# Performance work log

Measured on AMD Instinct MI355X. Metric: run time of the kernel, lower is better.

Reference implementation:

```python
import jax, jax.numpy as jnp
import numpy as np
from jax import lax

E = 20          # num experts / classes
BN_EPS = 1e-5


def _conv(x, w, b=None):
    # NCHW conv, stride 1, 'same' padding (kernel 3x3 or 1x1)
    y = lax.conv_general_dilated(x, w, (1, 1), 'SAME',
                                 dimension_numbers=('NCHW', 'OIHW', 'NCHW'))
    return y if b is None else y + b[None, :, None, None]


def _lrelu(x):
    return jnp.where(x >= 0, x, 0.2 * x)


def _bn(x, g, b, m, v):
    # inference-mode batchnorm
    scale = g * lax.rsqrt(v + BN_EPS)
    return x * scale[None, :, None, None] + (b - m * scale)[None, :, None, None]


def setup_inputs() -> dict:
    key = jax.random.key(0)
    ks = iter(jax.random.split(key, 40))
    def w(shape):
        return jax.random.normal(next(ks), shape, jnp.float32) * 0.05
    d = {}
    d['x'] = jax.random.normal(next(ks), (2, 3, 192, 192), jnp.float32)
    d['noise'] = jax.random.normal(next(ks), (2, 128, 192, 192), jnp.float32)
    # classification head
    d['cls_w1'] = w((64, 3, 3, 3));    d['cls_b1'] = jnp.zeros((64,), jnp.float32)
    d['cls_w2'] = w((128, 64, 3, 3));  d['cls_b2'] = jnp.zeros((128,), jnp.float32)
    d['cls_w3'] = w((256, 128, 3, 3)); d['cls_b3'] = jnp.zeros((256,), jnp.float32)
    d['cls_w4'] = w((512, 256, 1, 1)); d['cls_b4'] = jnp.zeros((512,), jnp.float32)
    d['cls_w5'] = w((E, 512, 1, 1));   d['cls_b5'] = jnp.zeros((E,), jnp.float32)
    for c, i in ((128, 1), (256, 2), (512, 3)):
        d[f'bn{i}_g'] = jnp.ones((c,), jnp.float32)
        d[f'bn{i}_b'] = jnp.zeros((c,), jnp.float32)
        d[f'bn{i}_m'] = jnp.zeros((c,), jnp.float32)
        d[f'bn{i}_v'] = jnp.ones((c,), jnp.float32)
    # 20 expert encoders (stacked on leading axis)
    d['enc_w1'] = w((E, 32, 3, 3, 3));    d['enc_b1'] = jnp.zeros((E, 32), jnp.float32)
    d['enc_w2'] = w((E, 64, 32, 3, 3));   d['enc_b2'] = jnp.zeros((E, 64), jnp.float32)
    d['enc_w3'] = w((E, 128, 64, 3, 3));  d['enc_b3'] = jnp.zeros((E, 128), jnp.float32)
    d['enc_w4'] = w((E, 128, 128, 3, 3)); d['enc_b4'] = jnp.zeros((E, 128), jnp.float32)
    # decoder (legacy=False: first two 1x1 convs have no bias)
    d['dec_w1'] = w((64, 128, 1, 1))
    d['dec_w2'] = w((32, 64, 1, 1))
    d['dec_w3'] = w((3, 32, 1, 1)); d['dec_b3'] = jnp.zeros((3,), jnp.float32)
    return d


def reference(x, noise,
              cls_w1, cls_b1, cls_w2, cls_b2, cls_w3, cls_b3,
              cls_w4, cls_b4, cls_w5, cls_b5,
              bn1_g, bn1_b, bn1_m, bn1_v,
              bn2_g, bn2_b, bn2_m, bn2_v,
              bn3_g, bn3_b, bn3_m, bn3_v,
              enc_w1, enc_b1, enc_w2, enc_b2, enc_w3, enc_b3, enc_w4, enc_b4,
              dec_w1, dec_w2, dec_w3, dec_b3):
    B, _, H, W = x.shape
    C = enc_w4.shape[1]  # 128
    # --- classification / routing ---
    h = _lrelu(_conv(x, cls_w1, cls_b1))
    h = _lrelu(_bn(_conv(h, cls_w2, cls_b2), bn1_g, bn1_b, bn1_m, bn1_v))
    h = _lrelu(_bn(_conv(h, cls_w3, cls_b3), bn2_g, bn2_b, bn2_m, bn2_v))
    h = _lrelu(_bn(_conv(h, cls_w4, cls_b4), bn3_g, bn3_b, bn3_m, bn3_v))
    classes = jax.nn.softmax(_conv(h, cls_w5, cls_b5), axis=1)  # [B,E,H,W]
    idx = jnp.argmax(classes, axis=1)  # [B,H,W] top-1 expert per pixel

    # --- run all 20 dense encoders (faithful to original torch.where masking) ---
    def enc(w1, b1, w2, b2, w3, b3, w4, b4):
        e = _lrelu(_conv(x, w1, b1))
        e = _lrelu(_conv(e, w2, b2))
        e = _lrelu(_conv(e, w3, b3))
        return _conv(e, w4, b4)
    embs = jax.vmap(enc)(enc_w1, enc_b1, enc_w2, enc_b2,
                         enc_w3, enc_b3, enc_w4, enc_b4)  # [E,B,128,H,W]
    embs = jnp.moveaxis(embs, 0, 1)  # [B,E,128,H,W]
    sel_idx = jnp.broadcast_to(idx[:, None, None, :, :], (B, 1, C, H, W))
    emb = jnp.take_along_axis(embs, sel_idx, axis=1)[:, 0]  # [B,128,H,W]

    # --- decode with additive noise ---
    d = _conv(emb + noise, dec_w1)
    d = _conv(d, dec_w2)
    out = _conv(d, dec_w3, dec_b3)  # [B,3,H,W]

    # --- load balancing loss ---
    one_hot = jax.nn.one_hot(idx, E, dtype=jnp.float32)          # [B,H,W,E]
    density = one_hot.reshape(B, -1, E).mean(axis=1)             # [B,E]
    density_proxy = classes.reshape(B, E, -1).mean(axis=-1)      # [B,E]
    lb = (density_proxy * density).mean() * float(E * E)
    return out, lb * 0.1
```

## Files before the change

kernel.cpp:

```cpp
#include <hip/hip_runtime.h>
#include <hip/hip_bf16.h>

typedef __hip_bfloat16 bf16;
typedef unsigned short u16;
typedef short s16x8 __attribute__((ext_vector_type(8)));
typedef float f32x4 __attribute__((ext_vector_type(4)));
#define MFMA16(a, b, c) __builtin_amdgcn_mfma_f32_16x16x32_bf16(a, b, c, 0, 0, 0)

#define HW_   36864
#define WP_   194
#define HWP_  37636
#define W_    192
#define SP_   9216

__device__ __forceinline__ float ldin(const void* p, size_t i, int f32) {
    return f32 ? ((const float*)p)[i] : __bfloat162float(((const bf16*)p)[i]);
}
__device__ __forceinline__ int probe_f32(const void* pr) {
    return ((const unsigned*)pr)[0] == 0x3F800000u;
}
__device__ __forceinline__ u16 f2bf(float f) {
    bf16 h = __float2bfloat16(f);
    return *reinterpret_cast<u16*>(&h);
}

__global__ __launch_bounds__(256) void pad_x_k(const void* __restrict__ x,
                                               float* __restrict__ xpad,
                                               const void* __restrict__ pr) {
    const int f32 = probe_f32(pr);
    int i = blockIdx.x * 256 + threadIdx.x;
    if (i >= 2 * 3 * HW_) return;
    int w = i % W_;
    int h = (i / W_) % W_;
    int c = i / HW_;
    xpad[(size_t)c * HWP_ + (size_t)(h + 1) * WP_ + (w + 1)] = ldin(x, i, f32);
}

__global__ __launch_bounds__(256) void conv3x3_k(
    const float* __restrict__ in, const void* __restrict__ wgt,
    const void* __restrict__ bias, const void* __restrict__ bng,
    const void* __restrict__ bnb, const void* __restrict__ bnm,
    const void* __restrict__ bnv, float* __restrict__ out,
    int Cin, int Cout, int lrelu, const void* __restrict__ pr)
{
    extern __shared__ float wl[];
    const int f32 = probe_f32(pr);
    const int tid = threadIdx.x;
    const int co0 = blockIdx.y * 8;
    const int b   = blockIdx.z;
    const int n = Cin * 72;
    for (int i = tid; i < n; i += 256) {
        int u = i & 7, r = i >> 3;
        int ci = r / 9, tap = r - ci * 9;
        wl[i] = ldin(wgt, ((size_t)(co0 + u) * Cin + ci) * 9 + tap, f32);
    }
    __syncthreads();

    const int pixb = blockIdx.x * 1024 + tid;
    int off[4];
#pragma unroll
    for (int p = 0; p < 4; ++p) {
        int pix = pixb + p * 256;
        int h = pix / W_, w = pix - h * W_;
        off[p] = (h + 1) * WP_ + (w + 1);
    }
    float acc[32];
#pragma unroll
    for (int i = 0; i < 32; ++i) acc[i] = 0.f;

    const int doff[9] = {-(WP_+1), -WP_, -(WP_-1), -1, 0, 1, WP_-1, WP_, WP_+1};
    const float* inb = in + (size_t)b * Cin * HWP_;
    for (int ci = 0; ci < Cin; ++ci) {
        const float* ip = inb + (size_t)ci * HWP_;
        const float* wp = wl + ci * 72;
#pragma unroll
        for (int tap = 0; tap < 9; ++tap) {
            const float4 wa = *(const float4*)(wp + tap * 8);
            const float4 wb = *(const float4*)(wp + tap * 8 + 4);
            const int d = doff[tap];
            float v[4];
#pragma unroll
            for (int p = 0; p < 4; ++p) v[p] = ip[off[p] + d];
#pragma unroll
            for (int p = 0; p < 4; ++p) {
                acc[p*8+0] += v[p] * wa.x;  acc[p*8+1] += v[p] * wa.y;
                acc[p*8+2] += v[p] * wa.z;  acc[p*8+3] += v[p] * wa.w;
                acc[p*8+4] += v[p] * wb.x;  acc[p*8+5] += v[p] * wb.y;
                acc[p*8+6] += v[p] * wb.z;  acc[p*8+7] += v[p] * wb.w;
            }
        }
    }

#pragma unroll
    for (int u = 0; u < 8; ++u) {
        const int co = co0 + u;
        float s = 1.f, t = 0.f;
        if (bng) {
            float g = ldin(bng, co, f32), bb = ldin(bnb, co, f32);
            float m = ldin(bnm, co, f32), vv = ldin(bnv, co, f32);
            s = g * rsqrtf(vv + 1e-5f);
            t = bb - m * s;
        }
        const float bs = bias ? ldin(bias, co, f32) : 0.f;
        float* op = out + ((size_t)b * Cout + co) * HWP_;
#pragma unroll
        for (int p = 0; p < 4; ++p) {
            float val = (acc[p*8+u] + bs) * s + t;
            if (lrelu) val = val >= 0.f ? val : 0.2f * val;
            op[off[p]] = val;
        }
    }
}

__global__ __launch_bounds__(256) void conv1x1s_k(
    const float* __restrict__ in, const void* __restrict__ wgt,
    const void* __restrict__ bias, const void* __restrict__ bng,
    const void* __restrict__ bnb, const void* __restrict__ bnm,
    const void* __restrict__ bnv, float* __restrict__ out,
    int Cin, int pix0, const void* __restrict__ pr)
{
    extern __shared__ float wl[];
    const int f32 = probe_f32(pr);
    const int tid = threadIdx.x;
    const int co0 = blockIdx.y * 8;
    const int b   = blockIdx.z;
    const int n = Cin * 8;
    for (int i = tid; i < n; i += 256) {
        int u = i & 7, ci = i >> 3;
        wl[i] = ldin(wgt, (size_t)(co0 + u) * Cin + ci, f32);
    }
    __syncthreads();

    const int pixb = pix0 + blockIdx.x * 1024 + tid;
    int off[4], lp[4];
#pragma unroll
    for (int p = 0; p < 4; ++p) {
        int pix = pixb + p * 256;
        lp[p] = pix - pix0;
        int h = pix / W_, w = pix - h * W_;
        off[p] = (h + 1) * WP_ + (w + 1);
    }
    float acc[32];
#pragma unroll
    for (int i = 0; i < 32; ++i) acc[i] = 0.f;

    for (int ci = 0; ci < Cin; ++ci) {
        const float* ip = in + ((size_t)b * Cin + ci) * HWP_;
        const float4 wa = *(const float4*)(wl + ci * 8);
        const float4 wb = *(const float4*)(wl + ci * 8 + 4);
        float v[4];
#pragma unroll
        for (int p = 0; p < 4; ++p) v[p] = ip[off[p]];
#pragma unroll
        for (int p = 0; p < 4; ++p) {
            acc[p*8+0] += v[p] * wa.x;  acc[p*8+1] += v[p] * wa.y;
            acc[p*8+2] += v[p] * wa.z;  acc[p*8+3] += v[p] * wa.w;
            acc[p*8+4] += v[p] * wb.x;  acc[p*8+5] += v[p] * wb.y;
            acc[p*8+6] += v[p] * wb.z;  acc[p*8+7] += v[p] * wb.w;
        }
    }

#pragma unroll
    for (int u = 0; u < 8; ++u) {
        const int co = co0 + u;
        float g = ldin(bng, co, f32), bb = ldin(bnb, co, f32);
        float m = ldin(bnm, co, f32), vv = ldin(bnv, co, f32);
        float s = g * rsqrtf(vv + 1e-5f);
        float t = bb - m * s;
        const float bs = ldin(bias, co, f32);
        float* op = out + ((size_t)b * 512 + co) * SP_;
#pragma unroll
        for (int p = 0; p < 4; ++p) {
            float val = (acc[p*8+u] + bs) * s + t;
            val = val >= 0.f ? val : 0.2f * val;
            op[lp[p]] = val;
        }
    }
}

__global__ __launch_bounds__(256) void heads_k(
    const float* __restrict__ c4q, const void* __restrict__ w5,
    const void* __restrict__ b5, int* __restrict__ idx,
    float* __restrict__ proxy, float* __restrict__ cntg, int pix0,
    const void* __restrict__ pr)
{
    extern __shared__ float wl[];
    __shared__ float sums[20];
    __shared__ float cnts[20];
    const int f32 = probe_f32(pr);
    const int tid = threadIdx.x;
    const int b = blockIdx.y;
    for (int i = tid; i < 512 * 20; i += 256) {
        int e = i % 20, ci = i / 20;
        wl[ci * 20 + e] = ldin(w5, (size_t)e * 512 + ci, f32);
    }
    if (tid < 20) { sums[tid] = 0.f; cnts[tid] = 0.f; }
    __syncthreads();

    const int lpix = blockIdx.x * 256 + tid;

    float acc[20];
#pragma unroll
    for (int e = 0; e < 20; ++e) acc[e] = ldin(b5, e, f32);
    const float* ip = c4q + (size_t)b * 512 * SP_;
    for (int ci = 0; ci < 512; ++ci) {
        const float v = ip[(size_t)ci * SP_ + lpix];
        const float* wp = wl + ci * 20;
#pragma unroll
        for (int e = 0; e < 20; ++e) acc[e] += v * wp[e];
    }

    float m = acc[0]; int am = 0;
#pragma unroll
    for (int e = 1; e < 20; ++e) if (acc[e] > m) { m = acc[e]; am = e; }
    float prb[20], ssum = 0.f;
#pragma unroll
    for (int e = 0; e < 20; ++e) { prb[e] = expf(acc[e] - m); ssum += prb[e]; }
    const float inv = 1.f / ssum;
    idx[b * HW_ + pix0 + lpix] = am;

    const int lane = tid & 63;
#pragma unroll
    for (int e = 0; e < 20; ++e) {
        float p = prb[e] * inv;
        p += __shfl_down(p, 32); p += __shfl_down(p, 16); p += __shfl_down(p, 8);
        p += __shfl_down(p, 4);  p += __shfl_down(p, 2);  p += __shfl_down(p, 1);
        if (lane == 0) atomicAdd(&sums[e], p);
        unsigned long long bal = __ballot(am == e);
        if (lane == 0) atomicAdd(&cnts[e], (float)__popcll(bal));
    }
    __syncthreads();
    if (tid < 20) {
        atomicAdd(&proxy[b * 20 + tid], sums[tid]);
        atomicAdd(&cntg[b * 20 + tid], cnts[tid]);
    }
}

__global__ __launch_bounds__(256) void wtx_k(const void* __restrict__ w,
                                             u16* __restrict__ wt,
                                             int Cout, int Cin, int nTot,
                                             const void* __restrict__ pr) {
    const int f32 = probe_f32(pr);
    int i = blockIdx.x * 256 + threadIdx.x;
    if (i >= nTot) return;
    int ci = i % Cin; int r = i / Cin;
    int co = r % Cout; r /= Cout;
    int tap = r % 9; int e = r / 9;
    size_t src = ((size_t)(e * Cout + co) * Cin + ci) * 9 + tap;
    wt[i] = f2bf(ldin(w, src, f32));
}

__global__ __launch_bounds__(512) void fused_expert_k(
    const float* __restrict__ xpad, const int* __restrict__ idx,
    const void* __restrict__ ew1, const void* __restrict__ eb1,
    const u16* __restrict__ Wt2, const void* __restrict__ eb2,
    const u16* __restrict__ Wt3, const void* __restrict__ eb3,
    const u16* __restrict__ Wt4, const void* __restrict__ eb4,
    float* __restrict__ emb, const void* __restrict__ pr)
{
    __shared__ __align__(16) char smem_[137216];
    u16*   e2s = (u16*)smem_;
    u16*   e3s = (u16*)(smem_ + 54272);
    u16*   e1s = (u16*)(smem_ + 54272);
    float* xs  = (float*)smem_;
    float* wl1 = (float*)(smem_ + 6912);
    u16*   w2s = (u16*)(smem_ + 86016);
    __shared__ int s_sel[256];
    __shared__ int s_wc[8];
    __shared__ unsigned long long s_selq[4];
    __shared__ u16 s_l3[324];
    __shared__ int s_c3;

    const int f32 = probe_f32(pr);
    const int tid  = threadIdx.x;
    const int lane = tid & 63, wv = tid >> 6;
    const int ml = lane & 15, q8 = (lane >> 4) * 8, m0 = (lane >> 4) * 4;
    const int b = blockIdx.y;
    const int eid = blockIdx.z;
    const int ty = blockIdx.x / 12, tx = blockIdx.x - ty * 12;
    const int Oh = ty * 16, Ow = tx * 16;

    {
        int sel = 0;
        if (tid < 256) {
            const int r = tid >> 4, c = tid & 15;
            sel = (idx[b * HW_ + (Oh + r) * W_ + (Ow + c)] == eid);
        }
        const unsigned long long m = __ballot(sel);
        if (lane == 0) {
            s_wc[wv] = __popcll(m);
            if (wv < 4) s_selq[wv] = m;
        }
        __syncthreads();
        int cnt = 0;
#pragma unroll
        for (int w = 0; w < 8; ++w) cnt += s_wc[w];
        if (cnt == 0) return;
        int pre = 0;
        for (int w = 0; w < wv; ++w) pre += s_wc[w];
        if (sel)
            s_sel[pre + __popcll(m & ((1ull << lane) - 1ull))] = tid;
    }

    if (wv == 0) {
        unsigned need = 0;
        const int r3 = lane;
        if (r3 < 18) {
            unsigned m = 0;
#pragma unroll
            for (int d = 0; d < 3; ++d) {
                const int r = r3 - 2 + d;
                if (r >= 0 && r < 16)
                    m |= (unsigned)((s_selq[r >> 2] >> ((r & 3) * 16)) & 0xFFFFull);
            }
            need = (m | (m << 1) | (m << 2)) & 0x3FFFFu;
        }
        const int pc = __popc(need);
        int inc = pc;
#pragma unroll
        for (int o = 1; o < 32; o <<= 1) {
            const int t = __shfl_up(inc, o);
            if (lane >= o) inc += t;
        }
        int k = inc - pc;
        unsigned mm = need;
        while (mm) {
            const int c = __ffs(mm) - 1;
            mm &= mm - 1;
            s_l3[k++] = (u16)(r3 * 18 + c);
        }
        if (lane == 17) s_c3 = inc;
    }

    for (int i = tid; i < 24 * 24 * 3; i += 512) {
        int ch = i % 3, pxl = i / 3;
        int r = pxl / 24, c = pxl - r * 24;
        int ir = Oh - 4 + r, ic = Ow - 4 + c;
        float v = 0.f;
        if (ir >= -1 && ir < 193 && ic >= -1 && ic < 193)
            v = xpad[((size_t)b * 3 + ch) * HWP_ + (size_t)(ir + 1) * WP_ + (ic + 1)];
        xs[pxl * 3 + ch] = v;
    }
    for (int i = tid; i < 896; i += 512) {
        if (i < 864) {
            int co = i & 31, k = i >> 5;
            int ci = k / 9, tap = k - ci * 9;
            wl1[i] = ldin(ew1, (size_t)eid * 864 + ((size_t)co * 3 + ci) * 9 + tap, f32);
        } else {
            wl1[i] = ldin(eb1, (size_t)eid * 32 + (i - 864), f32);
        }
    }
    {
        const u16* Wt2e = Wt2 + (size_t)eid * 9 * 64 * 32;
        for (int i = tid; i < 2304; i += 512) {
            int r = i >> 2, part = i & 3;
            *(uint4*)(w2s + (size_t)r * 40 + part * 8) =
                *(const uint4*)(Wt2e + (size_t)r * 32 + part * 8);
        }
    }
    __syncthreads();

    if (tid < 484) {
        const int p = tid;
        const int r1 = p / 22, c1 = p - r1 * 22;
        const int ir = Oh - 3 + r1, ic = Ow - 3 + c1;
        const int inimg = (ir >= 0 && ir < 192 && ic >= 0 && ic < 192);
        float a1[32];
#pragma unroll
        for (int co = 0; co < 32; ++co) a1[co] = 0.f;
        if (inimg) {
#pragma unroll
            for (int ci = 0; ci < 3; ++ci)
#pragma unroll
                for (int tap = 0; tap < 9; ++tap) {
                    const int dy = tap / 3, dx = tap - dy * 3;
                    const float xv = xs[((r1 + dy) * 24 + (c1 + dx)) * 3 + ci];
                    const float* wp = wl1 + (ci * 9 + tap) * 32;
#pragma unroll
                    for (int co = 0; co < 32; ++co) a1[co] += xv * wp[co];
                }
        }
        u16 pk[32];
#pragma unroll
        for (int co = 0; co < 32; ++co) {
            float v = 0.f;
            if (inimg) {
                v = a1[co] + wl1[864 + co];
                v = v >= 0.f ? v : 0.2f * v;
            }
            pk[co] = f2bf(v);
        }
#pragma unroll
        for (int ch = 0; ch < 4; ++ch)
            *(uint4*)(e1s + ((size_t)ch * 488 + p) * 8) = ((const uint4*)pk)[ch];
    }
    __syncthreads();

    {
        int pxv[4], r2v[4], c2v[4];
#pragma unroll
        for (int j = 0; j < 4; ++j) {
            int t = wv + 8 * j; if (t > 24) t = 24;
            int px = t * 16 + ml;
            pxv[j] = px; r2v[j] = px / 20; c2v[j] = px - (px / 20) * 20;
        }
        f32x4 acc2[4][4];
#pragma unroll
        for (int j = 0; j < 4; ++j)
#pragma unroll
            for (int n = 0; n < 4; ++n) acc2[j][n] = (f32x4){0.f,0.f,0.f,0.f};

#pragma unroll
        for (int tap = 0; tap < 9; ++tap) {
            const int dy = tap / 3, dx = tap - dy * 3;
            s16x8 aW[4];
#pragma unroll
            for (int n = 0; n < 4; ++n)
                aW[n] = *(const s16x8*)(w2s + ((size_t)tap * 64 + n * 16 + ml) * 40 + q8);
#pragma unroll
            for (int j = 0; j < 4; ++j) {
                const int lin = (r2v[j] + dy) * 22 + (c2v[j] + dx);
                const s16x8 bA = *(const s16x8*)(e1s + ((size_t)(q8 >> 3) * 488 + lin) * 8);
#pragma unroll
                for (int n = 0; n < 4; ++n) acc2[j][n] = MFMA16(aW[n], bA, acc2[j][n]);
            }
        }
        __syncthreads();
#pragma unroll
        for (int j = 0; j < 4; ++j) {
            const int px = pxv[j];
            const int r2 = r2v[j], c2 = c2v[j];
            const int ir = Oh - 2 + r2, ic = Ow - 2 + c2;
            const int inimg = (ir >= 0 && ir < 192 && ic >= 0 && ic < 192);
#pragma unroll
            for (int n = 0; n < 4; ++n) {
                u16 pk[4];
#pragma unroll
                for (int r = 0; r < 4; ++r) {
                    const int co = n * 16 + m0 + r;
                    float v = 0.f;
                    if (inimg) {
                        v = acc2[j][n][r] + ldin(eb2, (size_t)eid * 64 + co, f32);
                        v = v >= 0.f ? v : 0.2f * v;
                    }
                    pk[r] = f2bf(v);
                }
                const int chunk = (n * 16 + m0) >> 3;
                *(uint2*)(e2s + ((size_t)chunk * 424 + px) * 8 + (m0 & 4)) = *(const uint2*)pk;
            }
        }
    }
    __syncthreads();

    {
        const u16* Wt3e = Wt3 + (size_t)eid * 9 * 128 * 64;
        const int np = wv >> 2;
        const int w4 = wv & 3;
        const int cnt3 = s_c3;
        const int tiles3 = (cnt3 + 15) >> 4;
        const int jc = (w4 < tiles3) ? ((tiles3 - w4 + 3) >> 2) : 0;
        int pxv[6], r3v[6], c3v[6];
#pragma unroll
        for (int j = 0; j < 6; ++j) {
            int li = (w4 + 4 * j) * 16 + ml;
            if (li >= cnt3) li = cnt3 - 1;
            const int px = s_l3[li];
            pxv[j] = px; r3v[j] = px / 18; c3v[j] = px - (px / 18) * 18;
        }
        f32x4 acc3[6][4];
#pragma unroll
        for (int j = 0; j < 6; ++j)
#pragma unroll
            for (int n = 0; n < 4; ++n) acc3[j][n] = (f32x4){0.f,0.f,0.f,0.f};

#define LW3(dst, g) { const int tp_ = (g) >> 1, cc_ = (g) & 1;                         \
    dst[0] = *(const s16x8*)(Wt3e + ((size_t)tp_*128 + np*64 +  0 + ml)*64 + cc_*32 + q8); \
    dst[1] = *(const s16x8*)(Wt3e + ((size_t)tp_*128 + np*64 + 16 + ml)*64 + cc_*32 + q8); \
    dst[2] = *(const s16x8*)(Wt3e + ((size_t)tp_*128 + np*64 + 32 + ml)*64 + cc_*32 + q8); \
    dst[3] = *(const s16x8*)(Wt3e + ((size_t)tp_*128 + np*64 + 48 + ml)*64 + cc_*32 + q8); }
#define C3GROUP(BUF, g) { const int tp_ = (g) >> 1, cc_ = (g) & 1;                     \
    const int dy_ = tp_ / 3, dx_ = tp_ - dy_ * 3;                                      \
    const int ch_ = cc_ * 4 + (q8 >> 3);                                               \
    _Pragma("unroll")                                                                  \
    for (int j = 0; j < 6; ++j) if (j < jc) {                                          \
        const int lin_ = (r3v[j] + dy_) * 20 + (c3v[j] + dx_);                         \
        const s16x8 bA_ = *(const s16x8*)(e2s + ((size_t)ch_ * 424 + lin_) * 8);       \
        acc3[j][0] = MFMA16(BUF[0], bA_, acc3[j][0]);                                  \
        acc3[j][1] = MFMA16(BUF[1], bA_, acc3[j][1]);                                  \
        acc3[j][2] = MFMA16(BUF[2], bA_, acc3[j][2]);                                  \
        acc3[j][3] = MFMA16(BUF[3], bA_, acc3[j][3]); } }

        s16x8 aA[4], aB[4];
        LW3(aA, 0);
#pragma unroll
        for (int g = 0; g < 18; g += 2) {
            LW3(aB, g + 1);
            C3GROUP(aA, g);
            if (g + 2 < 18) LW3(aA, g + 2);
            C3GROUP(aB, g + 1);
        }
#undef LW3
#undef C3GROUP

        float b3[4][4];
#pragma unroll
        for (int n = 0; n < 4; ++n)
#pragma unroll
            for (int r = 0; r < 4; ++r)
                b3[n][r] = ldin(eb3, (size_t)eid * 128 + np * 64 + n * 16 + m0 + r, f32);
#pragma unroll
        for (int j = 0; j < 6; ++j) {
            if (j >= jc) continue;
            const int px = pxv[j];
            const int r3 = r3v[j], c3 = c3v[j];
            const int ir = Oh - 1 + r3, ic = Ow - 1 + c3;
            const int inimg = (ir >= 0 && ir < 192 && ic >= 0 && ic < 192);
#pragma unroll
            for (int n = 0; n < 4; ++n) {
                u16 pk[4];
#pragma unroll
                for (int r = 0; r < 4; ++r) {
                    float v = 0.f;
                    if (inimg) {
                        v = acc3[j][n][r] + b3[n][r];
                        v = v >= 0.f ? v : 0.2f * v;
                    }
                    pk[r] = f2bf(v);
                }
                const int chunk = (np * 64 + n * 16 + m0) >> 3;
                *(uint2*)(e3s + ((size_t)chunk * 324 + px) * 8 + (m0 & 4)) = *(const uint2*)pk;
            }
        }
    }
    __syncthreads();

    {
        const u16* Wt4e = Wt4 + (size_t)eid * 9 * 128 * 128;
        int cnt = 0;
#pragma unroll
        for (int w = 0; w < 8; ++w) cnt += s_wc[w];
        const int mtiles = (cnt + 15) >> 4;
        const int n0 = wv * 16;
        float bs[4];
#pragma unroll
        for (int r = 0; r < 4; ++r) bs[r] = ldin(eb4, (size_t)eid * 128 + n0 + m0 + r, f32);

#define LW4(dst, g) { const int tp_ = (g) >> 2, c0_ = ((g) & 3) * 32;                  \
    dst = *(const s16x8*)(Wt4e + ((size_t)tp_ * 128 + n0 + ml) * 128 + c0_ + q8); }
#define C4GROUP(BUF, g) { const int tp_ = (g) >> 2, cq_ = ((g) & 3) * 32 + q8;         \
    const int dy_ = tp_ / 3, dx_ = tp_ - dy_ * 3;                                      \
    const size_t cb_ = (size_t)(cq_ >> 3) * 324;                                       \
    _Pragma("unroll")                                                                  \
    for (int u = 0; u < 4; ++u) if (u < mc) {                                          \
        const int lin_ = (rrv[u] + dy_) * 18 + (ccv[u] + dx_);                         \
        const s16x8 bA_ = *(const s16x8*)(e3s + (cb_ + lin_) * 8);                     \
        acc4[u] = MFMA16(BUF, bA_, acc4[u]); } }

        for (int mt0 = 0; mt0 < mtiles; mt0 += 4) {
            const int mc = (mtiles - mt0 < 4) ? (mtiles - mt0) : 4;
            int rrv[4], ccv[4], liv[4];
#pragma unroll
            for (int u = 0; u < 4; ++u) {
                const int li = (mt0 + u) * 16 + ml;
                int lc = li; if (lc >= cnt) lc = cnt - 1;
                const int lpx = s_sel[lc];
                liv[u] = li; rrv[u] = lpx >> 4; ccv[u] = lpx & 15;
            }
            f32x4 acc4[4];
#pragma unroll
            for (int u = 0; u < 4; ++u) acc4[u] = (f32x4){0.f,0.f,0.f,0.f};

            s16x8 wA, wB, wC, wD;
            LW4(wA, 0); LW4(wB, 1);
#pragma unroll
            for (int g = 0; g < 36; g += 4) {
                LW4(wC, g + 2);
                LW4(wD, g + 3);
                C4GROUP(wA, g);
                C4GROUP(wB, g + 1);
                if (g + 4 < 36) LW4(wA, g + 4);
                if (g + 5 < 36) LW4(wB, g + 5);
                C4GROUP(wC, g + 2);
                C4GROUP(wD, g + 3);
            }
#pragma unroll
            for (int u = 0; u < 4; ++u) {
                if (u < mc && liv[u] < cnt) {
                    const int g2 = (Oh + rrv[u]) * W_ + Ow + ccv[u];
#pragma unroll
                    for (int r = 0; r < 4; ++r)
                        emb[((size_t)b * 128 + n0 + m0 + r) * HW_ + g2] = acc4[u][r] + bs[r];
                }
            }
        }
#undef LW4
#undef C4GROUP
    }
}

__global__ __launch_bounds__(256) void dec_fused_k(
    const float* __restrict__ emb, const void* __restrict__ noise,
    const void* __restrict__ dw1, const void* __restrict__ dw2,
    const void* __restrict__ dw3, const void* __restrict__ db3,
    void* __restrict__ outb, const void* __restrict__ pr)
{
    __shared__ float w1s[128 * 64];
    __shared__ float w2s[64 * 32];
    __shared__ float w3s[100];
    const int f32 = probe_f32(pr);
    const int tid = threadIdx.x;
    for (int i = tid; i < 128 * 64; i += 256) {
        int ci = i >> 6, co = i & 63;
        w1s[i] = ldin(dw1, (size_t)co * 128 + ci, f32);
    }
    for (int i = tid; i < 64 * 32; i += 256) {
        int ci = i >> 5, co = i & 31;
        w2s[i] = ldin(dw2, (size_t)co * 64 + ci, f32);
    }
    if (tid < 96) {
        int ci = tid / 3, k = tid - ci * 3;
        w3s[ci * 3 + k] = ldin(dw3, (size_t)k * 32 + ci, f32);
    }
    if (tid >= 96 && tid < 99) w3s[96 + tid - 96] = ldin(db3, tid - 96, f32);
    __syncthreads();

    const int b = blockIdx.y;
    const int pix = blockIdx.x * 256 + tid;

    float h1[64];
#pragma unroll
    for (int i = 0; i < 64; ++i) h1[i] = 0.f;
    for (int ci = 0; ci < 128; ++ci) {
        const size_t base = ((size_t)b * 128 + ci) * HW_ + pix;
        const float v = emb[base] + ldin(noise, base, f32);
        const float* wp = w1s + ci * 64;
#pragma unroll
        for (int c4 = 0; c4 < 16; ++c4) {
            const float4 w = *(const float4*)(wp + c4 * 4);
            h1[c4*4+0] += v * w.x; h1[c4*4+1] += v * w.y;
            h1[c4*4+2] += v * w.z; h1[c4*4+3] += v * w.w;
        }
    }
    float h2[32];
#pragma unroll
    for (int i = 0; i < 32; ++i) h2[i] = 0.f;
#pragma unroll
    for (int ci = 0; ci < 64; ++ci) {
        const float v = h1[ci];
        const float* wp = w2s + ci * 32;
#pragma unroll
        for (int c4 = 0; c4 < 8; ++c4) {
            const float4 w = *(const float4*)(wp + c4 * 4);
            h2[c4*4+0] += v * w.x; h2[c4*4+1] += v * w.y;
            h2[c4*4+2] += v * w.z; h2[c4*4+3] += v * w.w;
        }
    }
    float a0 = w3s[96], a1 = w3s[97], a2 = w3s[98];
#pragma unroll
    for (int ci = 0; ci < 32; ++ci) {
        const float v = h2[ci];
        a0 += v * w3s[ci * 3 + 0];
        a1 += v * w3s[ci * 3 + 1];
        a2 += v * w3s[ci * 3 + 2];
    }
    const size_t o0 = (size_t)(b * 3 + 0) * HW_ + pix;
    const size_t o1 = (size_t)(b * 3 + 1) * HW_ + pix;
    const size_t o2 = (size_t)(b * 3 + 2) * HW_ + pix;
    if (f32) {
        ((float*)outb)[o0] = a0; ((float*)outb)[o1] = a1; ((float*)outb)[o2] = a2;
    } else {
        ((bf16*)outb)[o0] = __float2bfloat16(a0);
        ((bf16*)outb)[o1] = __float2bfloat16(a1);
        ((bf16*)outb)[o2] = __float2bfloat16(a2);
    }
}

__global__ void lb_k(const float* __restrict__ proxy, const float* __restrict__ cnt,
                     void* __restrict__ out, const void* __restrict__ pr) {
    const int f32 = probe_f32(pr);
    const int t = threadIdx.x;
    const float inv = 1.0f / (float)HW_;
    float v = 0.f;
    if (t < 40) v = (proxy[t] * inv) * (cnt[t] * inv);
#pragma unroll
    for (int o = 32; o > 0; o >>= 1) v += __shfl_down(v, o);
    if (t == 0) {
        if (f32) ((float*)out)[221184] = v;
        else     ((bf16*)out)[221184] = __float2bfloat16(v);
    }
}

extern "C" void kernel_launch(void* const* d_in, const int* in_sizes, int n_in,
                              void* d_out, int out_size, void* d_ws, size_t ws_size,
                              hipStream_t stream) {
    (void)in_sizes; (void)n_in; (void)out_size; (void)ws_size;
    const void* x    = d_in[0];
    const void* noise= d_in[1];
    const void* cw1  = d_in[2];  const void* cb1 = d_in[3];
    const void* cw2  = d_in[4];  const void* cb2 = d_in[5];
    const void* cw3  = d_in[6];  const void* cb3 = d_in[7];
    const void* cw4  = d_in[8];  const void* cb4 = d_in[9];
    const void* cw5  = d_in[10]; const void* cb5 = d_in[11];
    const void* bn1g = d_in[12]; const void* bn1b = d_in[13];
    const void* bn1m = d_in[14]; const void* bn1v = d_in[15];
    const void* bn2g = d_in[16]; const void* bn2b = d_in[17];
    const void* bn2m = d_in[18]; const void* bn2v = d_in[19];
    const void* bn3g = d_in[20]; const void* bn3b = d_in[21];
    const void* bn3m = d_in[22]; const void* bn3v = d_in[23];
    const void* ew1  = d_in[24]; const void* eb1 = d_in[25];
    const void* ew2  = d_in[26]; const void* eb2 = d_in[27];
    const void* ew3  = d_in[28]; const void* eb3 = d_in[29];
    const void* ew4  = d_in[30]; const void* eb4 = d_in[31];
    const void* dw1  = d_in[32];
    const void* dw2  = d_in[33];
    const void* dw3  = d_in[34]; const void* db3 = d_in[35];
    const void* pr   = bn1v;

    char* ws = (char*)d_ws;
    constexpr size_t SZ_XPAD = (((size_t)2*3*HWP_*4) + 255) & ~(size_t)255;
    constexpr size_t O_BUF2  = SZ_XPAD;
    constexpr size_t SZ_BUF2 = (size_t)2*256*HWP_*4;
    constexpr size_t O_BUF1  = O_BUF2 + SZ_BUF2;
    constexpr size_t SZ_BUF1 = (size_t)2*128*HWP_*4;
    constexpr size_t O_IDX   = O_BUF1 + SZ_BUF1;
    constexpr size_t O_STAT  = O_IDX + (size_t)2*HW_*4;
    constexpr size_t WS_USED = O_STAT + 512;

    float* xpad  = (float*)(ws);
    float* buf2  = (float*)(ws + O_BUF2);
    int*   idx   = (int*)  (ws + O_IDX);
    float* proxy = (float*)(ws + O_STAT);
    float* cntg  = proxy + 40;

    float* c1  = buf2;
    float* c3  = buf2;
    float* c2  = (float*)(ws + O_BUF1);
    float* c4q = (float*)(ws + O_BUF1);
    float* emb = buf2;
    u16* Wt2 = (u16*)(ws + O_BUF1);
    u16* Wt3 = Wt2 + 368640;
    u16* Wt4 = Wt3 + 1474560;

    hipMemsetAsync(d_ws, 0, WS_USED, stream);

    dim3 blk(256);
    pad_x_k<<<dim3((2*3*HW_ + 255)/256), blk, 0, stream>>>(x, xpad, pr);

    conv3x3_k<<<dim3(36,  8, 2), blk,   3*288, stream>>>(xpad, cw1, cb1, nullptr,nullptr,nullptr,nullptr, c1,   3,  64, 1, pr);
    conv3x3_k<<<dim3(36, 16, 2), blk,  64*288, stream>>>(c1,   cw2, cb2, bn1g,bn1b,bn1m,bn1v,           c2,  64, 128, 1, pr);
    conv3x3_k<<<dim3(36, 32, 2), blk, 128*288, stream>>>(c2,   cw3, cb3, bn2g,bn2b,bn2m,bn2v,           c3, 128, 256, 1, pr);
    for (int s = 0; s < 4; ++s) {
        conv1x1s_k<<<dim3(9, 64, 2), blk, 256*32, stream>>>(c3, cw4, cb4, bn3g,bn3b,bn3m,bn3v, c4q, 256, s*SP_, pr);
        heads_k<<<dim3(36, 2), blk, 512*20*4, stream>>>(c4q, cw5, cb5, idx, proxy, cntg, s*SP_, pr);
    }

    wtx_k<<<dim3(1440),  blk, 0, stream>>>(ew2, Wt2,  64,  32,  368640, pr);
    wtx_k<<<dim3(5760),  blk, 0, stream>>>(ew3, Wt3, 128,  64, 1474560, pr);
    wtx_k<<<dim3(11520), blk, 0, stream>>>(ew4, Wt4, 128, 128, 2949120, pr);

    fused_expert_k<<<dim3(144, 2, 20), dim3(512), 0, stream>>>(
        xpad, idx, ew1, eb1, Wt2, eb2, Wt3, eb3, Wt4, eb4, emb, pr);

    dec_fused_k<<<dim3(144, 2), blk, 0, stream>>>(emb, noise, dw1, dw2, dw3, db3, d_out, pr);
    lb_k<<<1, 64, 0, stream>>>(proxy, cntg, d_out, pr);
}
```

Baseline: 2.508 ms.

## Fuse 1x1 conv and classifier head, retile 3x3 convs to 16 channels

```diff
diff --git a/kernel.cpp b/kernel.cpp
--- a/kernel.cpp
+++ b/kernel.cpp
@@ -11,7 +11,6 @@
 #define WP_   194
 #define HWP_  37636
 #define W_    192
-#define SP_   9216
 
 __device__ __forceinline__ float ldin(const void* p, size_t i, int f32) {
     return f32 ? ((const float*)p)[i] : __bfloat162float(((const bf16*)p)[i]);
@@ -46,20 +45,20 @@
     extern __shared__ float wl[];
     const int f32 = probe_f32(pr);
     const int tid = threadIdx.x;
-    const int co0 = blockIdx.y * 8;
+    const int co0 = blockIdx.y * 16;
     const int b   = blockIdx.z;
-    const int n = Cin * 72;
+    const int n = Cin * 144;
     for (int i = tid; i < n; i += 256) {
-        int u = i & 7, r = i >> 3;
+        int u = i & 15, r = i >> 4;
         int ci = r / 9, tap = r - ci * 9;
         wl[i] = ldin(wgt, ((size_t)(co0 + u) * Cin + ci) * 9 + tap, f32);
     }
     __syncthreads();
 
-    const int pixb = blockIdx.x * 1024 + tid;
-    int off[4];
-#pragma unroll
-    for (int p = 0; p < 4; ++p) {
+    const int pixb = blockIdx.x * 512 + tid;
+    int off[2];
+#pragma unroll
+    for (int p = 0; p < 2; ++p) {
         int pix = pixb + p * 256;
         int h = pix / W_, w = pix - h * W_;
         off[p] = (h + 1) * WP_ + (w + 1);
@@ -72,27 +71,33 @@
     const float* inb = in + (size_t)b * Cin * HWP_;
     for (int ci = 0; ci < Cin; ++ci) {
         const float* ip = inb + (size_t)ci * HWP_;
-        const float* wp = wl + ci * 72;
+        const float* wp = wl + ci * 144;
 #pragma unroll
         for (int tap = 0; tap < 9; ++tap) {
-            const float4 wa = *(const float4*)(wp + tap * 8);
-            const float4 wb = *(const float4*)(wp + tap * 8 + 4);
+            const float4 wa = *(const float4*)(wp + tap * 16);
+            const float4 wb = *(const float4*)(wp + tap * 16 + 4);
+            const float4 wc = *(const float4*)(wp + tap * 16 + 8);
+            const float4 wd = *(const float4*)(wp + tap * 16 + 12);
             const int d = doff[tap];
-            float v[4];
-#pragma unroll
-            for (int p = 0; p < 4; ++p) v[p] = ip[off[p] + d];
-#pragma unroll
-            for (int p = 0; p < 4; ++p) {
-                acc[p*8+0] += v[p] * wa.x;  acc[p*8+1] += v[p] * wa.y;
-                acc[p*8+2] += v[p] * wa.z;  acc[p*8+3] += v[p] * wa.w;
-                acc[p*8+4] += v[p] * wb.x;  acc[p*8+5] += v[p] * wb.y;
-                acc[p*8+6] += v[p] * wb.z;  acc[p*8+7] += v[p] * wb.w;
-            }
-        }
-    }
-
-#pragma unroll
-    for (int u = 0; u < 8; ++u) {
+            float v[2];
+#pragma unroll
+            for (int p = 0; p < 2; ++p) v[p] = ip[off[p] + d];
+#pragma unroll
+            for (int p = 0; p < 2; ++p) {
+                acc[p*16+ 0] += v[p] * wa.x;  acc[p*16+ 1] += v[p] * wa.y;
+                acc[p*16+ 2] += v[p] * wa.z;  acc[p*16+ 3] += v[p] * wa.w;
+                acc[p*16+ 4] += v[p] * wb.x;  acc[p*16+ 5] += v[p] * wb.y;
+                acc[p*16+ 6] += v[p] * wb.z;  acc[p*16+ 7] += v[p] * wb.w;
+                acc[p*16+ 8] += v[p] * wc.x;  acc[p*16+ 9] += v[p] * wc.y;
+                acc[p*16+10] += v[p] * wc.z;  acc[p*16+11] += v[p] * wc.w;
+                acc[p*16+12] += v[p] * wd.x;  acc[p*16+13] += v[p] * wd.y;
+                acc[p*16+14] += v[p] * wd.z;  acc[p*16+15] += v[p] * wd.w;
+            }
+        }
+    }
+
+#pragma unroll
+    for (int u = 0; u < 16; ++u) {
         const int co = co0 + u;
         float s = 1.f, t = 0.f;
         if (bng) {
@@ -104,120 +109,92 @@
         const float bs = bias ? ldin(bias, co, f32) : 0.f;
         float* op = out + ((size_t)b * Cout + co) * HWP_;
 #pragma unroll
-        for (int p = 0; p < 4; ++p) {
-            float val = (acc[p*8+u] + bs) * s + t;
+        for (int p = 0; p < 2; ++p) {
+            float val = (acc[p*16+u] + bs) * s + t;
             if (lrelu) val = val >= 0.f ? val : 0.2f * val;
             op[off[p]] = val;
         }
     }
 }
 
-__global__ __launch_bounds__(256) void conv1x1s_k(
-    const float* __restrict__ in, const void* __restrict__ wgt,
-    const void* __restrict__ bias, const void* __restrict__ bng,
+__global__ __launch_bounds__(128) __attribute__((amdgpu_waves_per_eu(4)))
+void c4head_k(
+    const float* __restrict__ c3, const void* __restrict__ w4,
+    const void* __restrict__ b4, const void* __restrict__ bng,
     const void* __restrict__ bnb, const void* __restrict__ bnm,
-    const void* __restrict__ bnv, float* __restrict__ out,
-    int Cin, int pix0, const void* __restrict__ pr)
-{
-    extern __shared__ float wl[];
-    const int f32 = probe_f32(pr);
-    const int tid = threadIdx.x;
-    const int co0 = blockIdx.y * 8;
-    const int b   = blockIdx.z;
-    const int n = Cin * 8;
-    for (int i = tid; i < n; i += 256) {
-        int u = i & 7, ci = i >> 3;
-        wl[i] = ldin(wgt, (size_t)(co0 + u) * Cin + ci, f32);
-    }
-    __syncthreads();
-
-    const int pixb = pix0 + blockIdx.x * 1024 + tid;
-    int off[4], lp[4];
-#pragma unroll
-    for (int p = 0; p < 4; ++p) {
-        int pix = pixb + p * 256;
-        lp[p] = pix - pix0;
-        int h = pix / W_, w = pix - h * W_;
-        off[p] = (h + 1) * WP_ + (w + 1);
-    }
-    float acc[32];
-#pragma unroll
-    for (int i = 0; i < 32; ++i) acc[i] = 0.f;
-
-    for (int ci = 0; ci < Cin; ++ci) {
-        const float* ip = in + ((size_t)b * Cin + ci) * HWP_;
-        const float4 wa = *(const float4*)(wl + ci * 8);
-        const float4 wb = *(const float4*)(wl + ci * 8 + 4);
-        float v[4];
-#pragma unroll
-        for (int p = 0; p < 4; ++p) v[p] = ip[off[p]];
-#pragma unroll
-        for (int p = 0; p < 4; ++p) {
-            acc[p*8+0] += v[p] * wa.x;  acc[p*8+1] += v[p] * wa.y;
-            acc[p*8+2] += v[p] * wa.z;  acc[p*8+3] += v[p] * wa.w;
-            acc[p*8+4] += v[p] * wb.x;  acc[p*8+5] += v[p] * wb.y;
-            acc[p*8+6] += v[p] * wb.z;  acc[p*8+7] += v[p] * wb.w;
-        }
-    }
-
-#pragma unroll
-    for (int u = 0; u < 8; ++u) {
-        const int co = co0 + u;
-        float g = ldin(bng, co, f32), bb = ldin(bnb, co, f32);
-        float m = ldin(bnm, co, f32), vv = ldin(bnv, co, f32);
-        float s = g * rsqrtf(vv + 1e-5f);
-        float t = bb - m * s;
-        const float bs = ldin(bias, co, f32);
-        float* op = out + ((size_t)b * 512 + co) * SP_;
-#pragma unroll
-        for (int p = 0; p < 4; ++p) {
-            float val = (acc[p*8+u] + bs) * s + t;
-            val = val >= 0.f ? val : 0.2f * val;
-            op[lp[p]] = val;
-        }
-    }
-}
-
-__global__ __launch_bounds__(256) void heads_k(
-    const float* __restrict__ c4q, const void* __restrict__ w5,
+    const void* __restrict__ bnv, const void* __restrict__ w5,
     const void* __restrict__ b5, int* __restrict__ idx,
-    float* __restrict__ proxy, float* __restrict__ cntg, int pix0,
+    float* __restrict__ proxy, float* __restrict__ cntg,
     const void* __restrict__ pr)
 {
-    extern __shared__ float wl[];
-    __shared__ float sums[20];
-    __shared__ float cnts[20];
+    __shared__ float wl4[256 * 32];
+    __shared__ float wl5[32 * 20];
+    __shared__ float sA[32], sT[32], sB[32];
+    __shared__ float sums[20], cnts[20];
     const int f32 = probe_f32(pr);
     const int tid = threadIdx.x;
     const int b = blockIdx.y;
-    for (int i = tid; i < 512 * 20; i += 256) {
-        int e = i % 20, ci = i / 20;
-        wl[ci * 20 + e] = ldin(w5, (size_t)e * 512 + ci, f32);
-    }
+    const int pix = blockIdx.x * 128 + tid;
+    const int h = pix / W_, w = pix - h * W_;
+    const int off = (h + 1) * WP_ + (w + 1);
     if (tid < 20) { sums[tid] = 0.f; cnts[tid] = 0.f; }
-    __syncthreads();
-
-    const int lpix = blockIdx.x * 256 + tid;
-
-    float acc[20];
-#pragma unroll
-    for (int e = 0; e < 20; ++e) acc[e] = ldin(b5, e, f32);
-    const float* ip = c4q + (size_t)b * 512 * SP_;
-    for (int ci = 0; ci < 512; ++ci) {
-        const float v = ip[(size_t)ci * SP_ + lpix];
-        const float* wp = wl + ci * 20;
-#pragma unroll
-        for (int e = 0; e < 20; ++e) acc[e] += v * wp[e];
-    }
-
-    float m = acc[0]; int am = 0;
-#pragma unroll
-    for (int e = 1; e < 20; ++e) if (acc[e] > m) { m = acc[e]; am = e; }
+
+    float acc20[20];
+#pragma unroll
+    for (int e = 0; e < 20; ++e) acc20[e] = ldin(b5, e, f32);
+
+    const float* ip = c3 + (size_t)b * 256 * HWP_ + off;
+
+    for (int ch = 0; ch < 16; ++ch) {
+        __syncthreads();
+        for (int i = tid; i < 256 * 32; i += 128) {
+            int u = i & 31, ci = i >> 5;
+            wl4[i] = ldin(w4, (size_t)(ch * 32 + u) * 256 + ci, f32);
+        }
+        for (int i = tid; i < 640; i += 128) {
+            int e = i % 20, u = i / 20;
+            wl5[u * 20 + e] = ldin(w5, (size_t)e * 512 + ch * 32 + u, f32);
+        }
+        if (tid < 32) {
+            const int co = ch * 32 + tid;
+            float g = ldin(bng, co, f32), bb = ldin(bnb, co, f32);
+            float m = ldin(bnm, co, f32), vv = ldin(bnv, co, f32);
+            float s = g * rsqrtf(vv + 1e-5f);
+            sA[tid] = s; sT[tid] = bb - m * s; sB[tid] = ldin(b4, co, f32);
+        }
+        __syncthreads();
+
+        float a32[32];
+#pragma unroll
+        for (int i = 0; i < 32; ++i) a32[i] = 0.f;
+        for (int ci = 0; ci < 256; ++ci) {
+            const float v = ip[(size_t)ci * HWP_];
+            const float* wp = wl4 + ci * 32;
+#pragma unroll
+            for (int c4_ = 0; c4_ < 8; ++c4_) {
+                const float4 ww = *(const float4*)(wp + c4_ * 4);
+                a32[c4_*4+0] += v * ww.x; a32[c4_*4+1] += v * ww.y;
+                a32[c4_*4+2] += v * ww.z; a32[c4_*4+3] += v * ww.w;
+            }
+        }
+#pragma unroll
+        for (int u = 0; u < 32; ++u) {
+            float val = (a32[u] + sB[u]) * sA[u] + sT[u];
+            val = val >= 0.f ? val : 0.2f * val;
+            const float* wp5 = wl5 + u * 20;
+#pragma unroll
+            for (int e = 0; e < 20; ++e) acc20[e] += val * wp5[e];
+        }
+    }
+
+    float m = acc20[0]; int am = 0;
+#pragma unroll
+    for (int e = 1; e < 20; ++e) if (acc20[e] > m) { m = acc20[e]; am = e; }
     float prb[20], ssum = 0.f;
 #pragma unroll
-    for (int e = 0; e < 20; ++e) { prb[e] = expf(acc[e] - m); ssum += prb[e]; }
+    for (int e = 0; e < 20; ++e) { prb[e] = expf(acc20[e] - m); ssum += prb[e]; }
     const float inv = 1.f / ssum;
-    idx[b * HW_ + pix0 + lpix] = am;
+    idx[b * HW_ + pix] = am;
 
     const int lane = tid & 63;
 #pragma unroll
@@ -426,6 +403,12 @@
             }
         }
         __syncthreads();
+        float b2r[4][4];
+#pragma unroll
+        for (int n = 0; n < 4; ++n)
+#pragma unroll
+            for (int r = 0; r < 4; ++r)
+                b2r[n][r] = ldin(eb2, (size_t)eid * 64 + n * 16 + m0 + r, f32);
 #pragma unroll
         for (int j = 0; j < 4; ++j) {
             const int px = pxv[j];
@@ -437,10 +420,9 @@
                 u16 pk[4];
 #pragma unroll
                 for (int r = 0; r < 4; ++r) {
-                    const int co = n * 16 + m0 + r;
                     float v = 0.f;
                     if (inimg) {
-                        v = acc2[j][n][r] + ldin(eb2, (size_t)eid * 64 + co, f32);
+                        v = acc2[j][n][r] + b2r[n][r];
                         v = v >= 0.f ? v : 0.2f * v;
                     }
                     pk[r] = f2bf(v);
@@ -735,7 +717,6 @@
     float* c1  = buf2;
     float* c3  = buf2;
     float* c2  = (float*)(ws + O_BUF1);
-    float* c4q = (float*)(ws + O_BUF1);
     float* emb = buf2;
     u16* Wt2 = (u16*)(ws + O_BUF1);
     u16* Wt3 = Wt2 + 368640;
@@ -746,13 +727,11 @@
     dim3 blk(256);
     pad_x_k<<<dim3((2*3*HW_ + 255)/256), blk, 0, stream>>>(x, xpad, pr);
 
-    conv3x3_k<<<dim3(36,  8, 2), blk,   3*288, stream>>>(xpad, cw1, cb1, nullptr,nullptr,nullptr,nullptr, c1,   3,  64, 1, pr);
-    conv3x3_k<<<dim3(36, 16, 2), blk,  64*288, stream>>>(c1,   cw2, cb2, bn1g,bn1b,bn1m,bn1v,           c2,  64, 128, 1, pr);
-    conv3x3_k<<<dim3(36, 32, 2), blk, 128*288, stream>>>(c2,   cw3, cb3, bn2g,bn2b,bn2m,bn2v,           c3, 128, 256, 1, pr);
-    for (int s = 0; s < 4; ++s) {
-        conv1x1s_k<<<dim3(9, 64, 2), blk, 256*32, stream>>>(c3, cw4, cb4, bn3g,bn3b,bn3m,bn3v, c4q, 256, s*SP_, pr);
-        heads_k<<<dim3(36, 2), blk, 512*20*4, stream>>>(c4q, cw5, cb5, idx, proxy, cntg, s*SP_, pr);
-    }
+    conv3x3_k<<<dim3(72,  4, 2), blk,   3*144*4, stream>>>(xpad, cw1, cb1, nullptr,nullptr,nullptr,nullptr, c1,   3,  64, 1, pr);
+    conv3x3_k<<<dim3(72,  8, 2), blk,  64*144*4, stream>>>(c1,   cw2, cb2, bn1g,bn1b,bn1m,bn1v,           c2,  64, 128, 1, pr);
+    conv3x3_k<<<dim3(72, 16, 2), blk, 128*144*4, stream>>>(c2,   cw3, cb3, bn2g,bn2b,bn2m,bn2v,           c3, 128, 256, 1, pr);
+    c4head_k<<<dim3(288, 2), dim3(128), 0, stream>>>(
+        c3, cw4, cb4, bn3g, bn3b, bn3m, bn3v, cw5, cb5, idx, proxy, cntg, pr);
 
     wtx_k<<<dim3(1440),  blk, 0, stream>>>(ew2, Wt2,  64,  32,  368640, pr);
     wtx_k<<<dim3(5760),  blk, 0, stream>>>(ew3, Wt3, 128,  64, 1474560, pr);
```

New measurement: 2.956 ms. 1.18x slower.
